# Kernel tuning notes

Hardware: AMD Instinct MI355X
Metric: run time of the kernel (lower is better)

## Reference

```python
import jax, jax.numpy as jnp
import numpy as np

GZ = 15          # grid size (gz)
C_IN = 4         # grid channels == R output dim
N_DEEP = 16      # number of stride-1 conv blocks after conv1
BN_EPS = 1e-5


def _bn_eval(x, g, b):
    # eval-mode BatchNorm2d with running_mean=0, running_var=1
    s = g / jnp.sqrt(1.0 + BN_EPS)
    return x * s[None, :, None, None] + b[None, :, None, None]


def _conv(x, w, b, stride):
    y = jax.lax.conv_general_dilated(
        x, w, window_strides=(stride, stride), padding=[(2, 2), (2, 2)],
        dimension_numbers=('NCHW', 'OIHW', 'NCHW'))
    return y + b[None, :, None, None]


def _cnn(x, conv1_w, conv1_b, bn1_g, bn1_b, convs_w, convs_b, bns_g, bns_b):
    x = jax.nn.elu(_bn_eval(_conv(x, conv1_w, conv1_b, 2), bn1_g, bn1_b))
    for i in range(N_DEEP):  # fixed small layer count
        x = jax.nn.elu(_bn_eval(_conv(x, convs_w[i], convs_b[i], 1), bns_g[i], bns_b[i]))
    return x


def _per_example_mean(points, attrs, W1, b1, W2, b2, W3, b3,
                      conv1_w, conv1_b, bn1_g, bn1_b, convs_w, convs_b, bns_g, bns_b):
    # Disty: scalar euclidean distance from each point to its cell center, + attr -> 2 features
    cell = jnp.clip(jnp.floor(points), 0.0, GZ - 1.0).astype(jnp.int32)  # [N,2]
    center = cell.astype(points.dtype) + 0.5
    dist = jnp.sqrt(jnp.sum((points - center) ** 2, axis=-1, keepdims=True) + 1e-12)  # [N,1]
    h = jnp.concatenate([dist, attrs], axis=-1)  # [N,2]
    # R: per-point MLP 2->16->16->4
    h = jax.nn.elu(h @ W1 + b1)
    h = jax.nn.elu(h @ W2 + b2)
    feats = h @ W3 + b3  # [N,4]
    # Agg: scatter-max into the 15x15 grid by containing cell
    cid = cell[:, 0] * GZ + cell[:, 1]  # [N]
    grid = jnp.zeros((GZ * GZ, C_IN), points.dtype).at[cid].max(feats)
    x = grid.reshape(GZ, GZ, C_IN).transpose(2, 0, 1)[None]  # [1,4,15,15]
    out = _cnn(x, conv1_w, conv1_b, bn1_g, bn1_b, convs_w, convs_b, bns_g, bns_b)
    return out.mean()


def setup_inputs():
    key = jax.random.key(0)
    ks = jax.random.split(key, 20)
    B, N = 128, 16384
    inp = {
        'points': jax.random.uniform(ks[0], (B, N, 2), jnp.float32) * GZ,
        'attrs': jax.random.normal(ks[1], (B, N, 1), jnp.float32),
        'goal_force': jax.random.normal(ks[2], (B, N, 2), jnp.float32) * 0.01,
        'goal_attrs': jax.random.normal(ks[3], (B, N, 1), jnp.float32) * 0.01,
    }
    def lin(k, i, o):
        return jax.random.normal(k, (i, o), jnp.float32) / np.float32(np.sqrt(i))
    inp['W1'] = lin(ks[4], 2, 16);  inp['b1'] = jnp.zeros((16,), jnp.float32)
    inp['W2'] = lin(ks[5], 16, 16); inp['b2'] = jnp.zeros((16,), jnp.float32)
    inp['W3'] = lin(ks[6], 16, 4);  inp['b3'] = jnp.zeros((4,), jnp.float32)
    inp['conv1_w'] = jax.random.normal(ks[7], (32, 4, 5, 5), jnp.float32) / np.float32(np.sqrt(4 * 25))
    inp['conv1_b'] = jnp.zeros((32,), jnp.float32)
    inp['bn1_g'] = jnp.ones((32,), jnp.float32)
    inp['bn1_b'] = jnp.zeros((32,), jnp.float32)
    inp['convs_w'] = jax.random.normal(ks[8], (N_DEEP, 32, 32, 5, 5), jnp.float32) / np.float32(np.sqrt(32 * 25))
    inp['convs_b'] = jnp.zeros((N_DEEP, 32), jnp.float32)
    inp['bns_g'] = jnp.ones((N_DEEP, 32), jnp.float32)
    inp['bns_b'] = jnp.zeros((N_DEEP, 32), jnp.float32)
    return inp


def reference(points, attrs, goal_force, goal_attrs, W1, b1, W2, b2, W3, b3,
              conv1_w, conv1_b, bn1_g, bn1_b, convs_w, convs_b, bns_g, bns_b):
    f = lambda p, a: _per_example_mean(p, a, W1, b1, W2, b2, W3, b3,
                                       conv1_w, conv1_b, bn1_g, bn1_b,
                                       convs_w, convs_b, bns_g, bns_b)
    # per-example gradient of output[idx].mean() wrt points/attrs (the torch autograd.grad loop)
    dpoints, dattrs = jax.vmap(jax.grad(f, argnums=(0, 1)))(points, attrs)
    cost = ((dpoints - goal_force) ** 2).mean() + ((dattrs - goal_attrs) ** 2).mean()
    B = points.shape[0]
    g_sum = (dpoints.sum() + dattrs.sum()) / B
    g_abs_sum = (jnp.abs(dpoints).sum() + jnp.abs(dattrs).sum()) / B
    return cost, g_sum, g_abs_sum, dpoints, dattrs
```

## Files before the change

kernel.cpp:

```cpp
#include <hip/hip_runtime.h>

#define TPB 256


static __device__ __forceinline__ unsigned long long dkey(double d) {
  unsigned long long b = (unsigned long long)__double_as_longlong(d);
  return (b & 0x8000000000000000ull) ? ~b : (b | 0x8000000000000000ull);
}

static __device__ __forceinline__ double expm1_fast(double z) {
  double t = z * 1.4426950408889634;
  double k = rint(t);
  double r = fma(k, -6.9314718036912381649e-01, z);
  r = fma(k, -1.9082149292705877e-10, r);
  double p = 2.08767569878681e-09;
  p = fma(p, r, 2.505210838544172e-08);
  p = fma(p, r, 2.755731922398589e-07);
  p = fma(p, r, 2.7557319223985893e-06);
  p = fma(p, r, 2.48015873015873e-05);
  p = fma(p, r, 1.984126984126984e-04);
  p = fma(p, r, 1.388888888888889e-03);
  p = fma(p, r, 8.333333333333333e-03);
  p = fma(p, r, 4.1666666666666664e-02);
  p = fma(p, r, 1.6666666666666666e-01);
  p = fma(p, r, 5e-01);
  double q = fma(r * p, r, r);
  long long ki = (long long)k;
  double s = __longlong_as_double((unsigned long long)(1023LL + ki) << 52);
  return fma(s, q, s - 1.0);
}

static __device__ __forceinline__ void mlp_forward(
    float px, float py, float at,
    const float* __restrict__ W1, const float* __restrict__ b1,
    const float* __restrict__ W2, const float* __restrict__ b2,
    const float* __restrict__ W3, const float* __restrict__ b3,
    int& c0, int& c1, double& dx, double& dy, double& dist,
    double a1[16], double a2[16], double f[4]) {
  c0 = (int)floorf(px); c0 = c0 < 0 ? 0 : (c0 > 14 ? 14 : c0);
  c1 = (int)floorf(py); c1 = c1 < 0 ? 0 : (c1 > 14 ? 14 : c1);
  dx = (double)px - ((double)c0 + 0.5);
  dy = (double)py - ((double)c1 + 0.5);
  dist = sqrt(fma(dx, dx, fma(dy, dy, 1e-12)));
  double datt = (double)at;
#pragma unroll
  for (int j = 0; j < 16; ++j) {
    double z = fma(dist, (double)W1[j], fma(datt, (double)W1[16 + j], (double)b1[j]));
    a1[j] = z > 0.0 ? z : expm1_fast(z);
  }
#pragma unroll
  for (int j = 0; j < 16; ++j) {
    double z = (double)b2[j];
#pragma unroll
    for (int i = 0; i < 16; ++i) z = fma(a1[i], (double)W2[i * 16 + j], z);
    a2[j] = z > 0.0 ? z : expm1_fast(z);
  }
#pragma unroll
  for (int k = 0; k < 4; ++k) {
    double ff = (double)b3[k];
#pragma unroll
    for (int i = 0; i < 16; ++i) ff = fma(a2[i], (double)W3[i * 4 + k], ff);
    f[k] = ff;
  }
}

__global__ __launch_bounds__(TPB)
void k_init(unsigned long long* __restrict__ gp) {
  int e = blockIdx.x * TPB + threadIdx.x;
  if (e < 128 * 900) gp[e] = 0x8000000000000000ull;
}

__global__ __launch_bounds__(TPB)
void k_wtrans(const float* __restrict__ cw, float* __restrict__ wT, float* __restrict__ wTb) {
  int i = blockIdx.x * TPB + threadIdx.x;
  if (i >= 409600) return;
  int c = i & 7;
  int m = (i >> 3) & 31;
  int g = (i >> 8) & 3;
  int jt = i >> 10;
  int t = jt % 25;
  int j = jt / 25;
  wT[i]  = cw[((size_t)(j * 32 + (g * 8 + c)) * 32 + m) * 25 + t];
  wTb[i] = cw[((size_t)(j * 32 + m) * 32 + (g * 8 + c)) * 25 + (24 - t)];
}

__global__ __launch_bounds__(TPB)
void k_scatter(const float* __restrict__ points, const float* __restrict__ attrs,
               const float* __restrict__ W1, const float* __restrict__ b1,
               const float* __restrict__ W2, const float* __restrict__ b2,
               const float* __restrict__ W3, const float* __restrict__ b3,
               unsigned long long* __restrict__ gp) {
  int gid = blockIdx.x * TPB + threadIdx.x;
  float2 p2 = ((const float2*)points)[gid];
  float at = attrs[gid];
  int c0, c1; double dx, dy, dist, a1[16], a2[16], f[4];
  mlp_forward(p2.x, p2.y, at, W1, b1, W2, b2, W3, b3, c0, c1, dx, dy, dist, a1, a2, f);
  int b = gid >> 14;
  unsigned long long inv = (unsigned long long)(16383 - (gid & 16383));
  size_t base = (size_t)b * 900 + (size_t)(c0 * 15 + c1) * 4;
#pragma unroll
  for (int k = 0; k < 4; ++k)
    atomicMax(&gp[base + k], (dkey(f[k]) & 0xFFFFFFFFFFFFC000ull) | inv);
}

static __device__ __forceinline__ void conv_mac8(const float* __restrict__ Rd, int rd_base,
                                                 const float* __restrict__ wb, float acc[8]) {
  int po = rd_base;
  const float* wp = wb;
#pragma unroll 1
  for (int ky = 0; ky < 5; ++ky) {
#pragma unroll 1
    for (int kx = 0; kx < 5; ++kx) {
      const float4 a0 = *(const float4*)&Rd[po];
      const float4 a1 = *(const float4*)&Rd[po + 4];
#pragma unroll
      for (int c = 0; c < 8; ++c) {
        acc[c] = fmaf(wp[c],      a0.x, acc[c]);
        acc[c] = fmaf(wp[8 + c],  a0.y, acc[c]);
        acc[c] = fmaf(wp[16 + c], a0.z, acc[c]);
        acc[c] = fmaf(wp[24 + c], a0.w, acc[c]);
        acc[c] = fmaf(wp[32 + c], a1.x, acc[c]);
        acc[c] = fmaf(wp[40 + c], a1.y, acc[c]);
        acc[c] = fmaf(wp[48 + c], a1.z, acc[c]);
        acc[c] = fmaf(wp[56 + c], a1.w, acc[c]);
      }
      po += 36; wp += 1024;
    }
    po += 7 * 36;
  }
}

__global__ __launch_bounds__(1024, 4)
void k_cnn(const unsigned long long* __restrict__ gp,
           const float* __restrict__ c1w, const float* __restrict__ c1b,
           const float* __restrict__ bn1g, const float* __restrict__ bn1b,
           const float* __restrict__ wT, const float* __restrict__ wTb,
           const float* __restrict__ cb, const float* __restrict__ bg,
           const float* __restrict__ bb,
           float* __restrict__ acts, float* __restrict__ dgrid) {
  __shared__ float xin[900];
  __shared__ __align__(16) float bufA[5184], bufB[5184];
  __shared__ __align__(16) float4 partA[768], partB[768];
  const int tid = threadIdx.x;
  const int b = blockIdx.x;
  for (int t = tid; t < 5184; t += 1024) { bufA[t] = 0.f; bufB[t] = 0.f; }
  if (tid < 900) {
    int c = tid / 225, rem = tid - c * 225;
    unsigned long long k = gp[(size_t)b * 900 + rem * 4 + c] & 0xFFFFFFFFFFFFC000ull;
    long long bits = (k & 0x8000000000000000ull) ? (long long)(k & 0x7FFFFFFFFFFFFFFFull)
                                                 : ~(long long)k;
    xin[c * 225 + rem] = (float)__longlong_as_double(bits);
  }
  __syncthreads();
  const float irs = 1.0f / sqrtf(1.0f + 1e-5f);
  float* actE = acts + (size_t)b * 34816;
#pragma unroll
  for (int r = 0; r < 2; ++r) {
    int k = tid + r * 1024;
    int co = k >> 6, pix = k & 63, y = pix >> 3, x = pix & 7;
    float acc = c1b[co];
    for (int ci = 0; ci < 4; ++ci)
#pragma unroll
      for (int ky = 0; ky < 5; ++ky) {
        int iy = 2 * y + ky - 2;
        if (iy < 0 || iy > 14) continue;
#pragma unroll
        for (int kx = 0; kx < 5; ++kx) {
          int ix = 2 * x + kx - 2;
          if (ix < 0 || ix > 14) continue;
          acc = fmaf(c1w[((co * 4 + ci) * 5 + ky) * 5 + kx], xin[ci * 225 + iy * 15 + ix], acc);
        }
      }
    float z = fmaf(acc, bn1g[co] * irs, bn1b[co]);
    float a = z > 0.f ? z : expm1f(z);
    bufA[((y + 2) * 12 + (x + 2)) * 36 + co] = a;
    actE[pix * 32 + co] = a;
  }
  __syncthreads();
  const int w = __builtin_amdgcn_readfirstlane(tid >> 6);
  const int lane = tid & 63;
  const int g = w & 3, q = w >> 2;
  const int y = lane >> 3, x = lane & 7;
  const int rd_base = (y * 12 + x) * 36 + q * 8;
  const int st_pix = ((y + 2) * 12 + (x + 2)) * 36 + g * 8;
#pragma unroll 1
  for (int j = 0; j < 16; ++j) {
    const float* Rd = (j & 1) ? bufB : bufA;
    float* Wr = (j & 1) ? bufA : bufB;
    const float* wb = wT + (size_t)j * 25600 + g * 256 + q * 64;
    float acc[8] = {0.f, 0.f, 0.f, 0.f, 0.f, 0.f, 0.f, 0.f};
    conv_mac8(Rd, rd_base, wb, acc);
    if (q > 0) {
      int slot = ((q - 1) * 4 + g) * 64 + lane;
      partA[slot] = make_float4(acc[0], acc[1], acc[2], acc[3]);
      partB[slot] = make_float4(acc[4], acc[5], acc[6], acc[7]);
    }
    __syncthreads();
    if (q == 0) {
#pragma unroll
      for (int p = 0; p < 3; ++p) {
        float4 pa = partA[(p * 4 + g) * 64 + lane];
        float4 pb = partB[(p * 4 + g) * 64 + lane];
        acc[0] += pa.x; acc[1] += pa.y; acc[2] += pa.z; acc[3] += pa.w;
        acc[4] += pb.x; acc[5] += pb.y; acc[6] += pb.z; acc[7] += pb.w;
      }
      const int cbase = j * 32 + g * 8;
      float av[8];
#pragma unroll
      for (int c = 0; c < 8; ++c) {
        float z = fmaf(acc[c] + cb[cbase + c], bg[cbase + c] * irs, bb[cbase + c]);
        av[c] = z > 0.f ? z : expm1f(z);
      }
      *(float4*)&Wr[st_pix]     = make_float4(av[0], av[1], av[2], av[3]);
      *(float4*)&Wr[st_pix + 4] = make_float4(av[4], av[5], av[6], av[7]);
      float* ap = actE + (size_t)(j + 1) * 2048 + lane * 32 + g * 8;
      *(float4*)&ap[0] = make_float4(av[0], av[1], av[2], av[3]);
      *(float4*)&ap[4] = make_float4(av[4], av[5], av[6], av[7]);
    }
    __syncthreads();
  }
#pragma unroll
  for (int r = 0; r < 2; ++r) {
    int t = tid + r * 1024;
    int ch = t & 31, pix = t >> 5;
    float a = actE[16 * 2048 + pix * 32 + ch];
    float d = (a > 0.f ? 1.f : a + 1.f) * (bg[15 * 32 + ch] * irs);
    bufA[((2 + (pix >> 3)) * 12 + 2 + (pix & 7)) * 36 + ch] = d * (1.0f / 2048.0f);
  }
  __syncthreads();
#pragma unroll 1
  for (int jj = 0; jj < 16; ++jj) {
    const int j = 15 - jj;
    const float* Gb = (jj & 1) ? bufB : bufA;
    float* Wr = (jj & 1) ? bufA : bufB;
    const float* wb = wTb + (size_t)j * 25600 + g * 256 + q * 64;
    float acc[8] = {0.f, 0.f, 0.f, 0.f, 0.f, 0.f, 0.f, 0.f};
    conv_mac8(Gb, rd_base, wb, acc);
    if (q > 0) {
      int slot = ((q - 1) * 4 + g) * 64 + lane;
      partA[slot] = make_float4(acc[0], acc[1], acc[2], acc[3]);
      partB[slot] = make_float4(acc[4], acc[5], acc[6], acc[7]);
    }
    __syncthreads();
    if (q == 0) {
#pragma unroll
      for (int p = 0; p < 3; ++p) {
        float4 pa = partA[(p * 4 + g) * 64 + lane];
        float4 pb = partB[(p * 4 + g) * 64 + lane];
        acc[0] += pa.x; acc[1] += pa.y; acc[2] += pa.z; acc[3] += pa.w;
        acc[4] += pb.x; acc[5] += pb.y; acc[6] += pb.z; acc[7] += pb.w;
      }
      const float* ap = actE + (size_t)j * 2048 + lane * 32 + g * 8;
      float4 A0 = *(const float4*)&ap[0];
      float4 A1 = *(const float4*)&ap[4];
      float avv[8] = {A0.x, A0.y, A0.z, A0.w, A1.x, A1.y, A1.z, A1.w};
#pragma unroll
      for (int c = 0; c < 8; ++c) {
        float s = (j > 0) ? bg[(j - 1) * 32 + g * 8 + c] : bn1g[g * 8 + c];
        acc[c] *= (avv[c] > 0.f ? 1.f : avv[c] + 1.f) * (s * irs);
      }
      *(float4*)&Wr[st_pix]     = make_float4(acc[0], acc[1], acc[2], acc[3]);
      *(float4*)&Wr[st_pix + 4] = make_float4(acc[4], acc[5], acc[6], acc[7]);
    }
    __syncthreads();
  }
  if (tid < 900) {
    int cid = tid >> 2, ci = tid & 3;
    int u = cid / 15, v = cid - u * 15;
    float acc = 0.f;
    for (int co = 0; co < 32; ++co) {
      const float* wp = c1w + (co * 4 + ci) * 25;
#pragma unroll
      for (int ky = 0; ky < 5; ++ky) {
        int t2 = u + 2 - ky;
        if (t2 < 0 || t2 > 14 || (t2 & 1)) continue;
        int yy = t2 >> 1;
#pragma unroll
        for (int kx = 0; kx < 5; ++kx) {
          int s2 = v + 2 - kx;
          if (s2 < 0 || s2 > 14 || (s2 & 1)) continue;
          int xq = s2 >> 1;
          acc = fmaf(wp[ky * 5 + kx], bufA[((yy + 2) * 12 + (xq + 2)) * 36 + co], acc);
        }
      }
    }
    dgrid[(size_t)b * 900 + tid] = acc;
  }
}

__global__ __launch_bounds__(TPB)
void k_winner(const float* __restrict__ points, const float* __restrict__ attrs,
              const float* __restrict__ W1, const float* __restrict__ b1,
              const float* __restrict__ W2, const float* __restrict__ b2,
              const float* __restrict__ W3, const float* __restrict__ b3,
              const unsigned long long* __restrict__ gp, const float* __restrict__ dgrid,
              float* __restrict__ dpoints, float* __restrict__ dattrs) {
  int e = blockIdx.x * TPB + threadIdx.x;
  unsigned long long pk = gp[e];
  if (pk <= 0x8000000000000000ull) return;
  float g = dgrid[e];
  if (g == 0.f) return;
  int b = e / 900;
  int r = e - b * 900;
  int ch = r & 3;
  int pi = 16383 - (int)(pk & 0x3FFFull);
  size_t pidx = ((size_t)b << 14) + pi;
  float px = points[2 * pidx], py = points[2 * pidx + 1], at = attrs[pidx];
  int c0, c1; double dx, dy, dist, a1[16], a2[16], f[4];
  mlp_forward(px, py, at, W1, b1, W2, b2, W3, b3, c0, c1, dx, dy, dist, a1, a2, f);
  double gz2[16];
#pragma unroll
  for (int i = 0; i < 16; ++i) {
    double ga2 = (double)g * (double)W3[i * 4 + ch];
    gz2[i] = ga2 * (a2[i] > 0.0 ? 1.0 : a2[i] + 1.0);
  }
  double gd = 0.0, gatt = 0.0;
#pragma unroll
  for (int i = 0; i < 16; ++i) {
    double ga1 = 0.0;
#pragma unroll
    for (int jj = 0; jj < 16; ++jj) ga1 = fma(gz2[jj], (double)W2[i * 16 + jj], ga1);
    double gz1 = ga1 * (a1[i] > 0.0 ? 1.0 : a1[i] + 1.0);
    gd = fma(gz1, (double)W1[i], gd);
    gatt = fma(gz1, (double)W1[16 + i], gatt);
  }
  double inv = 1.0 / dist;
  atomicAdd(&dpoints[2 * pidx], (float)(gd * dx * inv));
  atomicAdd(&dpoints[2 * pidx + 1], (float)(gd * dy * inv));
  atomicAdd(&dattrs[pidx], (float)gatt);
}

__global__ __launch_bounds__(TPB)
void k_reduce(const float* __restrict__ dpoints, const float* __restrict__ dattrs,
              const float* __restrict__ gforce, const float* __restrict__ gattr,
              float* __restrict__ out) {
  int i = blockIdx.x * TPB + threadIdx.x;
  float dp0 = dpoints[2 * i], dp1 = dpoints[2 * i + 1], da = dattrs[i];
  float gf0 = gforce[2 * i], gf1 = gforce[2 * i + 1], ga = gattr[i];
  float e0 = dp0 - gf0, e1 = dp1 - gf1, e2 = da - ga;
  float c1v = e0 * e0 + e1 * e1;
  float c2v = e2 * e2;
  float sm = dp0 + dp1 + da;
  float ab = fabsf(dp0) + fabsf(dp1) + fabsf(da);
#pragma unroll
  for (int o = 32; o > 0; o >>= 1) {
    c1v += __shfl_down(c1v, o, 64);
    c2v += __shfl_down(c2v, o, 64);
    sm += __shfl_down(sm, o, 64);
    ab += __shfl_down(ab, o, 64);
  }
  __shared__ float red[4][4];
  int wv = threadIdx.x >> 6, ln = threadIdx.x & 63;
  if (ln == 0) { red[wv][0] = c1v; red[wv][1] = c2v; red[wv][2] = sm; red[wv][3] = ab; }
  __syncthreads();
  if (threadIdx.x == 0) {
    float C1 = 0, C2 = 0, S = 0, A = 0;
    for (int w = 0; w < 4; ++w) { C1 += red[w][0]; C2 += red[w][1]; S += red[w][2]; A += red[w][3]; }
    atomicAdd(&out[0], C1 * (1.0f / 4194304.0f) + C2 * (1.0f / 2097152.0f));
    atomicAdd(&out[1], S * (1.0f / 128.0f));
    atomicAdd(&out[2], A * (1.0f / 128.0f));
  }
}

extern "C" void kernel_launch(void* const* d_in, const int* in_sizes, int n_in,
                              void* d_out, int out_size, void* d_ws, size_t ws_size,
                              hipStream_t stream) {
  (void)in_sizes; (void)n_in; (void)ws_size;
  const float* points = (const float*)d_in[0];
  const float* attrs  = (const float*)d_in[1];
  const float* gforce = (const float*)d_in[2];
  const float* gattr  = (const float*)d_in[3];
  const float* W1 = (const float*)d_in[4];
  const float* b1 = (const float*)d_in[5];
  const float* W2 = (const float*)d_in[6];
  const float* b2 = (const float*)d_in[7];
  const float* W3 = (const float*)d_in[8];
  const float* b3 = (const float*)d_in[9];
  const float* c1w  = (const float*)d_in[10];
  const float* c1b  = (const float*)d_in[11];
  const float* bn1g = (const float*)d_in[12];
  const float* bn1b = (const float*)d_in[13];
  const float* cw = (const float*)d_in[14];
  const float* cb = (const float*)d_in[15];
  const float* bg = (const float*)d_in[16];
  const float* bb = (const float*)d_in[17];
  float* out = (float*)d_out;

  char* ws = (char*)d_ws;
  unsigned long long* gp = (unsigned long long*)(ws);
  float* dgrid = (float*)(ws + 921600);
  float* wT  = (float*)(ws + 1382400);
  float* wTb = (float*)(ws + 3020800);
  float* acts = (float*)(ws + 4659200);

  float* dpoints = out + 3;
  float* dattrs  = out + 3 + 4194304;

  hipMemsetAsync(d_out, 0, (size_t)out_size * sizeof(float), stream);
  k_init<<<450, TPB, 0, stream>>>(gp);
  k_wtrans<<<1600, TPB, 0, stream>>>(cw, wT, wTb);
  k_scatter<<<8192, TPB, 0, stream>>>(points, attrs, W1, b1, W2, b2, W3, b3, gp);
  k_cnn<<<128, 1024, 0, stream>>>(gp, c1w, c1b, bn1g, bn1b, wT, wTb, cb, bg, bb, acts, dgrid);
  k_winner<<<450, TPB, 0, stream>>>(points, attrs, W1, b1, W2, b2, W3, b3, gp, dgrid,
                                    dpoints, dattrs);
  k_reduce<<<8192, TPB, 0, stream>>>(dpoints, dattrs, gforce, gattr, out);
}
```

Measured before the change: 1.212 ms.

## Spread conv split-K reduction across all waves and batch LDS loads per kernel row

The CNN conv loop previously had only the q==0 waves reduce partial sums and run the BN/ELU epilogue while the other three quarters of the block sat idle. Now every wave writes its partials to a larger shared array and all 16 waves each reduce and finish two output channels. conv_mac8 also loads all five kx activation vectors for a row up front to give more memory-level parallelism. The scatter kernel handles two points per thread with half the grid. The changes raise LDS use and register pressure, which could lower occupancy.

New measurement: 1.280 ms. 5.6% more time.

```diff
diff --git a/kernel.cpp b/kernel.cpp
--- a/kernel.cpp
+++ b/kernel.cpp
@@ -90,17 +90,21 @@
                const float* __restrict__ W2, const float* __restrict__ b2,
                const float* __restrict__ W3, const float* __restrict__ b3,
                unsigned long long* __restrict__ gp) {
-  int gid = blockIdx.x * TPB + threadIdx.x;
-  float2 p2 = ((const float2*)points)[gid];
-  float at = attrs[gid];
-  int c0, c1; double dx, dy, dist, a1[16], a2[16], f[4];
-  mlp_forward(p2.x, p2.y, at, W1, b1, W2, b2, W3, b3, c0, c1, dx, dy, dist, a1, a2, f);
-  int b = gid >> 14;
-  unsigned long long inv = (unsigned long long)(16383 - (gid & 16383));
-  size_t base = (size_t)b * 900 + (size_t)(c0 * 15 + c1) * 4;
-#pragma unroll
-  for (int k = 0; k < 4; ++k)
-    atomicMax(&gp[base + k], (dkey(f[k]) & 0xFFFFFFFFFFFFC000ull) | inv);
+  int idx = blockIdx.x * TPB + threadIdx.x;
+#pragma unroll
+  for (int r = 0; r < 2; ++r) {
+    int gid = idx + r * 1048576;
+    float2 p2 = ((const float2*)points)[gid];
+    float at = attrs[gid];
+    int c0, c1; double dx, dy, dist, a1[16], a2[16], f[4];
+    mlp_forward(p2.x, p2.y, at, W1, b1, W2, b2, W3, b3, c0, c1, dx, dy, dist, a1, a2, f);
+    int b = gid >> 14;
+    unsigned long long inv = (unsigned long long)(16383 - (gid & 16383));
+    size_t base = (size_t)b * 900 + (size_t)(c0 * 15 + c1) * 4;
+#pragma unroll
+    for (int k = 0; k < 4; ++k)
+      atomicMax(&gp[base + k], (dkey(f[k]) & 0xFFFFFFFFFFFFC000ull) | inv);
+  }
 }
 
 static __device__ __forceinline__ void conv_mac8(const float* __restrict__ Rd, int rd_base,
@@ -109,24 +113,30 @@
   const float* wp = wb;
 #pragma unroll 1
   for (int ky = 0; ky < 5; ++ky) {
-#pragma unroll 1
+    float4 a[10];
+#pragma unroll
     for (int kx = 0; kx < 5; ++kx) {
-      const float4 a0 = *(const float4*)&Rd[po];
-      const float4 a1 = *(const float4*)&Rd[po + 4];
+      a[2 * kx]     = *(const float4*)&Rd[po + kx * 36];
+      a[2 * kx + 1] = *(const float4*)&Rd[po + kx * 36 + 4];
+    }
+#pragma unroll
+    for (int kx = 0; kx < 5; ++kx) {
+      const float* w16 = wp + kx * 1024;
+      const float4 a0 = a[2 * kx], a1 = a[2 * kx + 1];
 #pragma unroll
       for (int c = 0; c < 8; ++c) {
-        acc[c] = fmaf(wp[c],      a0.x, acc[c]);
-        acc[c] = fmaf(wp[8 + c],  a0.y, acc[c]);
-        acc[c] = fmaf(wp[16 + c], a0.z, acc[c]);
-        acc[c] = fmaf(wp[24 + c], a0.w, acc[c]);
-        acc[c] = fmaf(wp[32 + c], a1.x, acc[c]);
-        acc[c] = fmaf(wp[40 + c], a1.y, acc[c]);
-        acc[c] = fmaf(wp[48 + c], a1.z, acc[c]);
-        acc[c] = fmaf(wp[56 + c], a1.w, acc[c]);
+        acc[c] = fmaf(w16[c],      a0.x, acc[c]);
+        acc[c] = fmaf(w16[8 + c],  a0.y, acc[c]);
+        acc[c] = fmaf(w16[16 + c], a0.z, acc[c]);
+        acc[c] = fmaf(w16[24 + c], a0.w, acc[c]);
+        acc[c] = fmaf(w16[32 + c], a1.x, acc[c]);
+        acc[c] = fmaf(w16[40 + c], a1.y, acc[c]);
+        acc[c] = fmaf(w16[48 + c], a1.z, acc[c]);
+        acc[c] = fmaf(w16[56 + c], a1.w, acc[c]);
       }
-      po += 36; wp += 1024;
-    }
-    po += 7 * 36;
+    }
+    po += 12 * 36;
+    wp += 5 * 1024;
   }
 }
 
@@ -140,7 +150,7 @@
            float* __restrict__ acts, float* __restrict__ dgrid) {
   __shared__ float xin[900];
   __shared__ __align__(16) float bufA[5184], bufB[5184];
-  __shared__ __align__(16) float4 partA[768], partB[768];
+  __shared__ __align__(16) float part[8192];
   const int tid = threadIdx.x;
   const int b = blockIdx.x;
   for (int t = tid; t < 5184; t += 1024) { bufA[t] = 0.f; bufB[t] = 0.f; }
@@ -182,7 +192,8 @@
   const int g = w & 3, q = w >> 2;
   const int y = lane >> 3, x = lane & 7;
   const int rd_base = (y * 12 + x) * 36 + q * 8;
-  const int st_pix = ((y + 2) * 12 + (x + 2)) * 36 + g * 8;
+  const int co2 = 2 * w;
+  const int ep_pix = ((y + 2) * 12 + (x + 2)) * 36 + co2;
 #pragma unroll 1
   for (int j = 0; j < 16; ++j) {
     const float* Rd = (j & 1) ? bufB : bufA;
@@ -190,32 +201,22 @@
     const float* wb = wT + (size_t)j * 25600 + g * 256 + q * 64;
     float acc[8] = {0.f, 0.f, 0.f, 0.f, 0.f, 0.f, 0.f, 0.f};
     conv_mac8(Rd, rd_base, wb, acc);
-    if (q > 0) {
-      int slot = ((q - 1) * 4 + g) * 64 + lane;
-      partA[slot] = make_float4(acc[0], acc[1], acc[2], acc[3]);
-      partB[slot] = make_float4(acc[4], acc[5], acc[6], acc[7]);
-    }
+#pragma unroll
+    for (int c = 0; c < 8; ++c)
+      part[((q * 32) + g * 8 + c) * 64 + lane] = acc[c];
     __syncthreads();
-    if (q == 0) {
-#pragma unroll
-      for (int p = 0; p < 3; ++p) {
-        float4 pa = partA[(p * 4 + g) * 64 + lane];
-        float4 pb = partB[(p * 4 + g) * 64 + lane];
-        acc[0] += pa.x; acc[1] += pa.y; acc[2] += pa.z; acc[3] += pa.w;
-        acc[4] += pb.x; acc[5] += pb.y; acc[6] += pb.z; acc[7] += pb.w;
-      }
-      const int cbase = j * 32 + g * 8;
-      float av[8];
-#pragma unroll
-      for (int c = 0; c < 8; ++c) {
-        float z = fmaf(acc[c] + cb[cbase + c], bg[cbase + c] * irs, bb[cbase + c]);
-        av[c] = z > 0.f ? z : expm1f(z);
-      }
-      *(float4*)&Wr[st_pix]     = make_float4(av[0], av[1], av[2], av[3]);
-      *(float4*)&Wr[st_pix + 4] = make_float4(av[4], av[5], av[6], av[7]);
-      float* ap = actE + (size_t)(j + 1) * 2048 + lane * 32 + g * 8;
-      *(float4*)&ap[0] = make_float4(av[0], av[1], av[2], av[3]);
-      *(float4*)&ap[4] = make_float4(av[4], av[5], av[6], av[7]);
+    {
+      float s0 = part[(0 * 32 + co2) * 64 + lane] + part[(1 * 32 + co2) * 64 + lane]
+               + part[(2 * 32 + co2) * 64 + lane] + part[(3 * 32 + co2) * 64 + lane];
+      float s1 = part[(0 * 32 + co2 + 1) * 64 + lane] + part[(1 * 32 + co2 + 1) * 64 + lane]
+               + part[(2 * 32 + co2 + 1) * 64 + lane] + part[(3 * 32 + co2 + 1) * 64 + lane];
+      const int cb0 = j * 32 + co2;
+      float z0 = fmaf(s0 + cb[cb0],     bg[cb0] * irs,     bb[cb0]);
+      float z1 = fmaf(s1 + cb[cb0 + 1], bg[cb0 + 1] * irs, bb[cb0 + 1]);
+      float a0 = z0 > 0.f ? z0 : expm1f(z0);
+      float a1v = z1 > 0.f ? z1 : expm1f(z1);
+      *(float2*)&Wr[ep_pix] = make_float2(a0, a1v);
+      *(float2*)&actE[(size_t)(j + 1) * 2048 + lane * 32 + co2] = make_float2(a0, a1v);
     }
     __syncthreads();
   }
@@ -236,31 +237,21 @@
     const float* wb = wTb + (size_t)j * 25600 + g * 256 + q * 64;
     float acc[8] = {0.f, 0.f, 0.f, 0.f, 0.f, 0.f, 0.f, 0.f};
     conv_mac8(Gb, rd_base, wb, acc);
-    if (q > 0) {
-      int slot = ((q - 1) * 4 + g) * 64 + lane;
-      partA[slot] = make_float4(acc[0], acc[1], acc[2], acc[3]);
-      partB[slot] = make_float4(acc[4], acc[5], acc[6], acc[7]);
-    }
+#pragma unroll
+    for (int c = 0; c < 8; ++c)
+      part[((q * 32) + g * 8 + c) * 64 + lane] = acc[c];
     __syncthreads();
-    if (q == 0) {
-#pragma unroll
-      for (int p = 0; p < 3; ++p) {
-        float4 pa = partA[(p * 4 + g) * 64 + lane];
-        float4 pb = partB[(p * 4 + g) * 64 + lane];
-        acc[0] += pa.x; acc[1] += pa.y; acc[2] += pa.z; acc[3] += pa.w;
-        acc[4] += pb.x; acc[5] += pb.y; acc[6] += pb.z; acc[7] += pb.w;
-      }
-      const float* ap = actE + (size_t)j * 2048 + lane * 32 + g * 8;
-      float4 A0 = *(const float4*)&ap[0];
-      float4 A1 = *(const float4*)&ap[4];
-      float avv[8] = {A0.x, A0.y, A0.z, A0.w, A1.x, A1.y, A1.z, A1.w};
-#pragma unroll
-      for (int c = 0; c < 8; ++c) {
-        float s = (j > 0) ? bg[(j - 1) * 32 + g * 8 + c] : bn1g[g * 8 + c];
-        acc[c] *= (avv[c] > 0.f ? 1.f : avv[c] + 1.f) * (s * irs);
-      }
-      *(float4*)&Wr[st_pix]     = make_float4(acc[0], acc[1], acc[2], acc[3]);
-      *(float4*)&Wr[st_pix + 4] = make_float4(acc[4], acc[5], acc[6], acc[7]);
+    {
+      float s0 = part[(0 * 32 + co2) * 64 + lane] + part[(1 * 32 + co2) * 64 + lane]
+               + part[(2 * 32 + co2) * 64 + lane] + part[(3 * 32 + co2) * 64 + lane];
+      float s1 = part[(0 * 32 + co2 + 1) * 64 + lane] + part[(1 * 32 + co2 + 1) * 64 + lane]
+               + part[(2 * 32 + co2 + 1) * 64 + lane] + part[(3 * 32 + co2 + 1) * 64 + lane];
+      float2 av = *(const float2*)&actE[(size_t)j * 2048 + lane * 32 + co2];
+      float sc0 = (j > 0) ? bg[(j - 1) * 32 + co2]     : bn1g[co2];
+      float sc1 = (j > 0) ? bg[(j - 1) * 32 + co2 + 1] : bn1g[co2 + 1];
+      s0 *= (av.x > 0.f ? 1.f : av.x + 1.f) * (sc0 * irs);
+      s1 *= (av.y > 0.f ? 1.f : av.y + 1.f) * (sc1 * irs);
+      *(float2*)&Wr[ep_pix] = make_float2(s0, s1);
     }
     __syncthreads();
   }
@@ -399,7 +390,7 @@
   hipMemsetAsync(d_out, 0, (size_t)out_size * sizeof(float), stream);
   k_init<<<450, TPB, 0, stream>>>(gp);
   k_wtrans<<<1600, TPB, 0, stream>>>(cw, wT, wTb);
-  k_scatter<<<8192, TPB, 0, stream>>>(points, attrs, W1, b1, W2, b2, W3, b3, gp);
+  k_scatter<<<4096, TPB, 0, stream>>>(points, attrs, W1, b1, W2, b2, W3, b3, gp);
   k_cnn<<<128, 1024, 0, stream>>>(gp, c1w, c1b, bn1g, bn1b, wT, wTb, cb, bg, bb, acts, dgrid);
   k_winner<<<450, TPB, 0, stream>>>(points, attrs, W1, b1, W2, b2, W3, b3, gp, dgrid,
                                     dpoints, dattrs);
```
